# Kernel optimization log

Measured on AMD Instinct MI355X. Metric: run time of the kernel, lower is better.

The kernel has to match this reference:

```python
import jax, jax.numpy as jnp
import numpy as np

BATCH, CHANNEL, LENGTH, CHI, D = 1024, 10, 784, 64, 2


def _dims():
    # dims[n+1] = min(d**(n+1), chi, d**(length-n-1)); dims[0] = 1
    dims = [1]
    for n in range(LENGTH):
        dims.append(min(D ** (n + 1), CHI, D ** (LENGTH - n - 1)))
    return dims


def _site_mask():
    # zero out tensor entries outside the [dims[n], dims[n+1]] bond block; this is
    # exactly equivalent to the per-site slicing in the torch code, but lets us
    # run one uniform lax.scan over sites with full-chi tensors.
    dims = _dims()
    mask = np.zeros((LENGTH, CHI, 1, CHI), np.float32)
    for n in range(LENGTH):
        mask[n, :dims[n], :, :dims[n + 1]] = 1.0
    return jnp.asarray(mask)


def setup_inputs() -> dict:
    key = jax.random.key(0)
    k1, k2 = jax.random.split(key)
    x = jax.random.uniform(k1, (BATCH, D, LENGTH), dtype=jnp.float32)
    scale = 1.0 / np.sqrt(CHI * D)
    tensors = jax.random.normal(k2, (CHANNEL, LENGTH, CHI, D, CHI), dtype=jnp.float32) * scale
    return {"x": x, "tensors": tensors}


def _forward(x, tensors):
    # mask == slicing tensors[:, nt, :dims[nt], :, :dims[nt+1]] at every site
    mt = tensors * _site_mask()[None]              # (c, L, chi, d, chi)
    A = jnp.transpose(mt, (1, 0, 2, 3, 4))         # (L, c, chi, d, chi)
    xs = jnp.transpose(x, (2, 0, 1))               # (L, n, d)
    is_last = jnp.arange(LENGTH) == LENGTH - 1
    y0 = jnp.zeros((x.shape[0], CHANNEL, CHI), x.dtype).at[:, :, 0].set(1.0)

    def step(y, inp):
        a, xv, last = inp
        y = jnp.einsum('nca,caib,ni->ncb', y, a, xv)
        # activation '(tanh(y)+1)/2' on all sites except the last one
        y = jnp.where(last, y, (jnp.tanh(y) + 1.0) * 0.5)
        return y, None

    y, _ = jax.lax.scan(step, y0, (A, xs, is_last))
    return y[:, :, :1]  # dims[length] == 1 -> (n, channel, 1)


def reference(x, tensors):
    return _forward(x, tensors)
```

## Files before the change

### kernel.cpp

```cpp
#include <hip/hip_runtime.h>
#include <hip/hip_bf16.h>


#define LEN 784
#define NCH 10

typedef short bf16x8 __attribute__((ext_vector_type(8)));
typedef float f32x4  __attribute__((ext_vector_type(4)));

#define WSA_SHORTS ((size_t)NCH * LEN * 8192)
#define WSX_FLOATS ((size_t)LEN * 2048)
#define WS_NEED (WSA_SHORTS * 2 + WSX_FLOATS * 4)

static __device__ __forceinline__ unsigned short f2bf(float f) {
    union { __hip_bfloat16 h; unsigned short s; } u;
    u.h = __float2bfloat16(f);
    return u.s;
}

__global__ __launch_bounds__(1024) void prepass(const float* __restrict__ x,
                                                const float* __restrict__ tens,
                                                short* __restrict__ wsA,
                                                float* __restrict__ wsX)
{
    const int bid = blockIdx.x;
    const int t = threadIdx.x;
    if (bid < NCH * LEN) {
        const int w = t >> 8, ii = (t >> 7) & 1, kf = (t >> 6) & 1, l = t & 63;
        const int bout = 16 * w + (l & 15);
        const int a0 = 32 * kf + 8 * (l >> 4);
        const float* src = tens + (size_t)bid * 8192;
        unsigned int wv[4];
        #pragma unroll
        for (int p = 0; p < 4; ++p) {
            float f0 = src[(size_t)(a0 + 2 * p) * 128 + ii * 64 + bout];
            float f1 = src[(size_t)(a0 + 2 * p + 1) * 128 + ii * 64 + bout];
            wv[p] = (unsigned)f2bf(f0) | ((unsigned)f2bf(f1) << 16);
        }
        *(int4*)(wsA + (size_t)bid * 8192 + (size_t)t * 8) = *(int4*)wv;
    } else {
        int n = bid - NCH * LEN;
        #pragma unroll
        for (int k = 0; k < 2; ++k) {
            int c2 = t + k * 1024;
            wsX[(size_t)n * 2048 + c2] =
                x[(size_t)(c2 >> 1) * (2 * LEN) + (size_t)(c2 & 1) * LEN + n];
        }
    }
}

template <bool USE_WS>
__global__ __launch_bounds__(256, 4) void mps_fwd4(const float* __restrict__ x,
                                                   const float* __restrict__ tens,
                                                   const short* __restrict__ wsA,
                                                   const float* __restrict__ wsX,
                                                   float* __restrict__ out)
{
    __shared__ short tbuf[2][1024];

    const int tid = threadIdx.x;
    const int lane = tid & 63;
    const int w = tid >> 6;
    const int g = lane >> 4, l15 = lane & 15;

    const int bid = blockIdx.x;
    const int ch = bid >> 6;
    const int b0 = (bid & 63) * 16;

    const short* asrc = wsA + (size_t)ch * LEN * 8192 + (size_t)w * 2048;
    const float* tsrc = tens + (size_t)ch * LEN * 8192;

    for (int idx = tid; idx < 1024; idx += 256) {
        int col = idx >> 6, a = idx & 63;
        tbuf[0][col * 64 + 8 * ((a >> 3) ^ (col & 7)) + (a & 7)] =
            (a == 0) ? (short)0x3F80 : (short)0;
    }

    int rd_off[2];
    #pragma unroll
    for (int kf = 0; kf < 2; ++kf)
        rd_off[kf] = l15 * 64 + 8 * ((4 * kf + g) ^ (l15 & 7));
    const int wr_off = l15 * 64 + 8 * ((2 * w + (g >> 1)) ^ (l15 & 7)) + 4 * (g & 1);

    auto load_afrags = [&](int site, bf16x8 (&A)[4]) {
        if (USE_WS) {
            const short* sb = asrc + (size_t)site * 8192;
            #pragma unroll
            for (int f = 0; f < 4; ++f)
                A[f] = *(const bf16x8*)(sb + f * 512 + lane * 8);
        } else {
            const float* sb = tsrc + (size_t)site * 8192;
            #pragma unroll
            for (int f = 0; f < 4; ++f) {
                int ii = f >> 1, kf = f & 1;
                int bout = 16 * w + l15;
                int a0 = 32 * kf + 8 * g;
                unsigned int wv[4];
                #pragma unroll
                for (int p = 0; p < 4; ++p) {
                    float f0 = sb[(size_t)(a0 + 2 * p) * 128 + ii * 64 + bout];
                    float f1 = sb[(size_t)(a0 + 2 * p + 1) * 128 + ii * 64 + bout];
                    wv[p] = (unsigned)f2bf(f0) | ((unsigned)f2bf(f1) << 16);
                }
                A[f] = *(bf16x8*)wv;
            }
        }
    };

    auto load_x = [&](int site, float2& xv) {
        if (USE_WS) {
            xv = *(const float2*)(wsX + (size_t)site * 2048 + 2 * (b0 + l15));
        } else {
            xv.x = x[(size_t)(b0 + l15) * (2 * LEN) + site];
            xv.y = x[(size_t)(b0 + l15) * (2 * LEN) + LEN + site];
        }
    };

    auto body = [&](int n, bf16x8 (&Acur)[4], bf16x8 (&Anxt)[4],
                    float2& xcur, float2& xnxt) {
        const int cur = n & 1, nxt = cur ^ 1;

        if (n + 1 < LEN) { load_afrags(n + 1, Anxt); load_x(n + 1, xnxt); }

        bf16x8 tf0 = *(const bf16x8*)&tbuf[cur][rd_off[0]];
        bf16x8 tf1 = *(const bf16x8*)&tbuf[cur][rd_off[1]];

        f32x4 acc0 = (f32x4){0.f, 0.f, 0.f, 0.f};
        f32x4 acc1 = (f32x4){0.f, 0.f, 0.f, 0.f};
        acc0 = __builtin_amdgcn_mfma_f32_16x16x32_bf16(Acur[0], tf0, acc0, 0, 0, 0);
        acc0 = __builtin_amdgcn_mfma_f32_16x16x32_bf16(Acur[1], tf1, acc0, 0, 0, 0);
        acc1 = __builtin_amdgcn_mfma_f32_16x16x32_bf16(Acur[2], tf0, acc1, 0, 0, 0);
        acc1 = __builtin_amdgcn_mfma_f32_16x16x32_bf16(Acur[3], tf1, acc1, 0, 0, 0);

        if (n == LEN - 1) {
            if (w == 0 && g == 0) {
                float v = xcur.x * acc0[0] + xcur.y * acc1[0];
                out[(size_t)(b0 + l15) * NCH + ch] = v;
            }
        } else {
            int e1 = (n + 1) < 6 ? (1 << (n + 1)) : 64;
            int e2 = (783 - n) < 6 ? (1 << (783 - n)) : 64;
            int dout = e1 < e2 ? e1 : e2;
            int abase = 16 * w + 4 * g;
            float xs0 = xcur.x * -2.88539008177792681f;
            float xs1 = xcur.y * -2.88539008177792681f;
            unsigned short sv[4];
            #pragma unroll
            for (int r = 0; r < 4; ++r) {
                float u = xs0 * acc0[r] + xs1 * acc1[r];
                float sg = __builtin_amdgcn_rcpf(1.0f + exp2f(u));
                sv[r] = (abase + r < dout) ? f2bf(sg) : (unsigned short)0;
            }
            int2 pk;
            pk.x = (int)((unsigned)sv[0] | ((unsigned)sv[1] << 16));
            pk.y = (int)((unsigned)sv[2] | ((unsigned)sv[3] << 16));
            *(int2*)&tbuf[nxt][wr_off] = pk;
        }
        __syncthreads();
    };

    bf16x8 A0[4], A1[4];
    float2 xv0, xv1;
    load_afrags(0, A0);
    load_x(0, xv0);
    __syncthreads();

    for (int n = 0; n < LEN; n += 2) {
        body(n, A0, A1, xv0, xv1);
        body(n + 1, A1, A0, xv1, xv0);
    }
}

extern "C" void kernel_launch(void* const* d_in, const int* in_sizes, int n_in,
                              void* d_out, int out_size, void* d_ws, size_t ws_size,
                              hipStream_t stream) {
    (void)in_sizes; (void)n_in; (void)out_size;
    const float* x    = (const float*)d_in[0];
    const float* tens = (const float*)d_in[1];
    float* out = (float*)d_out;
    if (ws_size >= WS_NEED) {
        short* wsA = (short*)d_ws;
        float* wsX = (float*)((char*)d_ws + WSA_SHORTS * 2);
        hipLaunchKernelGGL(prepass, dim3(NCH * LEN + LEN), dim3(1024), 0, stream,
                           x, tens, wsA, wsX);
        hipLaunchKernelGGL((mps_fwd4<true>), dim3(640), dim3(256), 0, stream,
                           x, tens, wsA, wsX, out);
    } else {
        hipLaunchKernelGGL((mps_fwd4<false>), dim3(640), dim3(256), 0, stream,
                           x, tens, (const short*)nullptr, (const float*)nullptr, out);
    }
}
```

Measured before the change: 610.5 us.

## Deepen A-fragment prefetch to two sites, batch x loads, remap blocks

Result: faster. 554.2 us (-9.2%).

```diff
diff --git a/kernel.cpp b/kernel.cpp
--- a/kernel.cpp
+++ b/kernel.cpp
@@ -9,8 +9,11 @@
 typedef float f32x4  __attribute__((ext_vector_type(4)));
 
 #define WSA_SHORTS ((size_t)NCH * LEN * 8192)
-#define WSX_FLOATS ((size_t)LEN * 2048)
+#define WSX_FLOATS ((size_t)1024 * 2 * LEN)
 #define WS_NEED (WSA_SHORTS * 2 + WSX_FLOATS * 4)
+
+#define XSCALE -2.88539008177792681f
+#define XUNDO  -0.34657359027997264f
 
 static __device__ __forceinline__ unsigned short f2bf(float f) {
     union { __hip_bfloat16 h; unsigned short s; } u;
@@ -39,18 +42,18 @@
         }
         *(int4*)(wsA + (size_t)bid * 8192 + (size_t)t * 8) = *(int4*)wv;
     } else {
-        int n = bid - NCH * LEN;
-        #pragma unroll
-        for (int k = 0; k < 2; ++k) {
-            int c2 = t + k * 1024;
-            wsX[(size_t)n * 2048 + c2] =
-                x[(size_t)(c2 >> 1) * (2 * LEN) + (size_t)(c2 & 1) * LEN + n];
+        int b = bid - NCH * LEN;
+        if (t < LEN) {
+            float v0 = x[(size_t)b * (2 * LEN) + t] * XSCALE;
+            float v1 = x[(size_t)b * (2 * LEN) + LEN + t] * XSCALE;
+            float2 pk; pk.x = v0; pk.y = v1;
+            *(float2*)(wsX + (size_t)b * (2 * LEN) + 2 * t) = pk;
         }
     }
 }
 
 template <bool USE_WS>
-__global__ __launch_bounds__(256, 4) void mps_fwd4(const float* __restrict__ x,
+__global__ __launch_bounds__(256, 3) void mps_fwd5(const float* __restrict__ x,
                                                    const float* __restrict__ tens,
                                                    const short* __restrict__ wsA,
                                                    const float* __restrict__ wsX,
@@ -63,12 +66,15 @@
     const int w = tid >> 6;
     const int g = lane >> 4, l15 = lane & 15;
 
-    const int bid = blockIdx.x;
-    const int ch = bid >> 6;
-    const int b0 = (bid & 63) * 16;
+    const int p = blockIdx.x;
+    const int gidx = (p & 7) * 80 + (p >> 3);
+    const int ch = gidx >> 6;
+    const int b0 = (gidx & 63) * 16;
 
     const short* asrc = wsA + (size_t)ch * LEN * 8192 + (size_t)w * 2048;
     const float* tsrc = tens + (size_t)ch * LEN * 8192;
+    const float* xsrc = USE_WS ? (wsX + (size_t)(b0 + l15) * (2 * LEN))
+                               : (x + (size_t)(b0 + l15) * (2 * LEN));
 
     for (int idx = tid; idx < 1024; idx += 256) {
         int col = idx >> 6, a = idx & 63;
@@ -76,13 +82,12 @@
             (a == 0) ? (short)0x3F80 : (short)0;
     }
 
-    int rd_off[2];
-    #pragma unroll
-    for (int kf = 0; kf < 2; ++kf)
-        rd_off[kf] = l15 * 64 + 8 * ((4 * kf + g) ^ (l15 & 7));
+    int rd_off0 = l15 * 64 + 8 * ((0 + g) ^ (l15 & 7));
+    int rd_off1 = l15 * 64 + 8 * ((4 + g) ^ (l15 & 7));
     const int wr_off = l15 * 64 + 8 * ((2 * w + (g >> 1)) ^ (l15 & 7)) + 4 * (g & 1);
 
-    auto load_afrags = [&](int site, bf16x8 (&A)[4]) {
+    auto loadA = [&](int site, bf16x8 (&A)[4]) {
+        site = site < LEN ? site : LEN - 1;
         if (USE_WS) {
             const short* sb = asrc + (size_t)site * 8192;
             #pragma unroll
@@ -97,44 +102,49 @@
                 int a0 = 32 * kf + 8 * g;
                 unsigned int wv[4];
                 #pragma unroll
-                for (int p = 0; p < 4; ++p) {
-                    float f0 = sb[(size_t)(a0 + 2 * p) * 128 + ii * 64 + bout];
-                    float f1 = sb[(size_t)(a0 + 2 * p + 1) * 128 + ii * 64 + bout];
-                    wv[p] = (unsigned)f2bf(f0) | ((unsigned)f2bf(f1) << 16);
+                for (int q2 = 0; q2 < 4; ++q2) {
+                    float f0 = sb[(size_t)(a0 + 2 * q2) * 128 + ii * 64 + bout];
+                    float f1 = sb[(size_t)(a0 + 2 * q2 + 1) * 128 + ii * 64 + bout];
+                    wv[q2] = (unsigned)f2bf(f0) | ((unsigned)f2bf(f1) << 16);
                 }
                 A[f] = *(bf16x8*)wv;
             }
         }
     };
 
-    auto load_x = [&](int site, float2& xv) {
+    auto loadX = [&](int nb, float4& qa, float4& qb) {
+        nb = nb <= LEN - 4 ? nb : LEN - 4;
         if (USE_WS) {
-            xv = *(const float2*)(wsX + (size_t)site * 2048 + 2 * (b0 + l15));
+            qa = *(const float4*)(xsrc + 2 * nb);
+            qb = *(const float4*)(xsrc + 2 * nb + 4);
         } else {
-            xv.x = x[(size_t)(b0 + l15) * (2 * LEN) + site];
-            xv.y = x[(size_t)(b0 + l15) * (2 * LEN) + LEN + site];
+            float4 xi0 = *(const float4*)(xsrc + nb);
+            float4 xi1 = *(const float4*)(xsrc + LEN + nb);
+            qa.x = xi0.x * XSCALE; qa.y = xi1.x * XSCALE;
+            qa.z = xi0.y * XSCALE; qa.w = xi1.y * XSCALE;
+            qb.x = xi0.z * XSCALE; qb.y = xi1.z * XSCALE;
+            qb.z = xi0.w * XSCALE; qb.w = xi1.w * XSCALE;
         }
     };
 
-    auto body = [&](int n, bf16x8 (&Acur)[4], bf16x8 (&Anxt)[4],
-                    float2& xcur, float2& xnxt) {
+    auto body = [&](int n, bf16x8 (&Ac)[4], bf16x8 (&Al)[4], float x0s, float x1s) {
         const int cur = n & 1, nxt = cur ^ 1;
 
-        if (n + 1 < LEN) { load_afrags(n + 1, Anxt); load_x(n + 1, xnxt); }
-
-        bf16x8 tf0 = *(const bf16x8*)&tbuf[cur][rd_off[0]];
-        bf16x8 tf1 = *(const bf16x8*)&tbuf[cur][rd_off[1]];
+        loadA(n + 2, Al);
+
+        bf16x8 tf0 = *(const bf16x8*)&tbuf[cur][rd_off0];
+        bf16x8 tf1 = *(const bf16x8*)&tbuf[cur][rd_off1];
 
         f32x4 acc0 = (f32x4){0.f, 0.f, 0.f, 0.f};
         f32x4 acc1 = (f32x4){0.f, 0.f, 0.f, 0.f};
-        acc0 = __builtin_amdgcn_mfma_f32_16x16x32_bf16(Acur[0], tf0, acc0, 0, 0, 0);
-        acc0 = __builtin_amdgcn_mfma_f32_16x16x32_bf16(Acur[1], tf1, acc0, 0, 0, 0);
-        acc1 = __builtin_amdgcn_mfma_f32_16x16x32_bf16(Acur[2], tf0, acc1, 0, 0, 0);
-        acc1 = __builtin_amdgcn_mfma_f32_16x16x32_bf16(Acur[3], tf1, acc1, 0, 0, 0);
+        acc0 = __builtin_amdgcn_mfma_f32_16x16x32_bf16(Ac[0], tf0, acc0, 0, 0, 0);
+        acc0 = __builtin_amdgcn_mfma_f32_16x16x32_bf16(Ac[1], tf1, acc0, 0, 0, 0);
+        acc1 = __builtin_amdgcn_mfma_f32_16x16x32_bf16(Ac[2], tf0, acc1, 0, 0, 0);
+        acc1 = __builtin_amdgcn_mfma_f32_16x16x32_bf16(Ac[3], tf1, acc1, 0, 0, 0);
 
         if (n == LEN - 1) {
             if (w == 0 && g == 0) {
-                float v = xcur.x * acc0[0] + xcur.y * acc1[0];
+                float v = (x0s * acc0[0] + x1s * acc1[0]) * XUNDO;
                 out[(size_t)(b0 + l15) * NCH + ch] = v;
             }
         } else {
@@ -142,12 +152,10 @@
             int e2 = (783 - n) < 6 ? (1 << (783 - n)) : 64;
             int dout = e1 < e2 ? e1 : e2;
             int abase = 16 * w + 4 * g;
-            float xs0 = xcur.x * -2.88539008177792681f;
-            float xs1 = xcur.y * -2.88539008177792681f;
             unsigned short sv[4];
             #pragma unroll
             for (int r = 0; r < 4; ++r) {
-                float u = xs0 * acc0[r] + xs1 * acc1[r];
+                float u = x0s * acc0[r] + x1s * acc1[r];
                 float sg = __builtin_amdgcn_rcpf(1.0f + exp2f(u));
                 sv[r] = (abase + r < dout) ? f2bf(sg) : (unsigned short)0;
             }
@@ -156,18 +164,25 @@
             pk.y = (int)((unsigned)sv[2] | ((unsigned)sv[3] << 16));
             *(int2*)&tbuf[nxt][wr_off] = pk;
         }
-        __syncthreads();
+
+        asm volatile("s_waitcnt lgkmcnt(0)\n\ts_barrier" ::: "memory");
     };
 
-    bf16x8 A0[4], A1[4];
-    float2 xv0, xv1;
-    load_afrags(0, A0);
-    load_x(0, xv0);
     __syncthreads();
 
-    for (int n = 0; n < LEN; n += 2) {
-        body(n, A0, A1, xv0, xv1);
-        body(n + 1, A1, A0, xv1, xv0);
+    bf16x8 As0[4], As1[4], As2[4], As3[4];
+    float4 xa, xb, xna, xnb;
+    loadA(0, As0);
+    loadA(1, As1);
+    loadX(0, xa, xb);
+
+    for (int nb = 0; nb < LEN; nb += 4) {
+        loadX(nb + 4, xna, xnb);
+        body(nb + 0, As0, As2, xa.x, xa.y);
+        body(nb + 1, As1, As3, xa.z, xa.w);
+        body(nb + 2, As2, As0, xb.x, xb.y);
+        body(nb + 3, As3, As1, xb.z, xb.w);
+        xa = xna; xb = xnb;
     }
 }
 
@@ -181,12 +196,12 @@
     if (ws_size >= WS_NEED) {
         short* wsA = (short*)d_ws;
         float* wsX = (float*)((char*)d_ws + WSA_SHORTS * 2);
-        hipLaunchKernelGGL(prepass, dim3(NCH * LEN + LEN), dim3(1024), 0, stream,
+        hipLaunchKernelGGL(prepass, dim3(NCH * LEN + 1024), dim3(1024), 0, stream,
                            x, tens, wsA, wsX);
-        hipLaunchKernelGGL((mps_fwd4<true>), dim3(640), dim3(256), 0, stream,
+        hipLaunchKernelGGL((mps_fwd5<true>), dim3(640), dim3(256), 0, stream,
                            x, tens, wsA, wsX, out);
     } else {
-        hipLaunchKernelGGL((mps_fwd4<false>), dim3(640), dim3(256), 0, stream,
+        hipLaunchKernelGGL((mps_fwd5<false>), dim3(640), dim3(256), 0, stream,
                            x, tens, (const short*)nullptr, (const float*)nullptr, out);
     }
 }
```
